# Performance work log

Measured on AMD Instinct MI355X. Metric: run time of the kernel, lower is better.

The kernel has to match this reference:

```python
import jax, jax.numpy as jnp
from jax import lax
import numpy as np

N3, N2, N1, N0 = 862, 1723, 3445, 6890  # mesh hierarchy (SMPL 6890 verts)
DEG, K = 16, 4  # nnz/row per Chebyshev support; K = order 3 + 1 supports


def _conv(x, w, b, s):
    y = lax.conv_general_dilated(x, w, (s, s), 'VALID', dimension_numbers=('NCHW', 'OIHW', 'NCHW'))
    return y + b[None, :, None, None]


def _pool(x):
    return lax.reduce_window(x, -jnp.inf, lax.max, (1, 1, 2, 2), (1, 1, 2, 2), 'VALID')


def _lin(x, w, b):
    return x @ w.T + b


def _rodrigues(r):  # [J,3] axis-angle -> [J,3,3] (batch_rodrigues)
    th = jnp.linalg.norm(r, axis=1, keepdims=True) + 1e-8
    k = r / th
    kx, ky, kz = k[:, 0], k[:, 1], k[:, 2]
    z = jnp.zeros_like(kx)
    Km = jnp.stack([z, -kz, ky, kz, z, -kx, -ky, kx, z], axis=1).reshape(-1, 3, 3)
    th = th[:, :, None]
    return jnp.eye(3, dtype=r.dtype)[None] + jnp.sin(th) * Km + (1.0 - jnp.cos(th)) * (Km @ Km)


def _spmm(idx, val, x):  # torch.sparse.mm with fixed nnz/row; idx,val: [N,D]
    return jnp.einsum('nd,ndf->nf', val, x[idx])


def _gcl(x, idx, val, W, b):  # Chebyshev graph conv: sum_k (A_k @ x) @ W_k + b
    return jnp.einsum('knd,kndf,kfo->no', val, x[idx], W) + b


def _basenet(frame, p):
    (c1w, c1b, c2w, c2b, c3w, c3b, c4w, c4b, c5w, c5b, fc1w, fc1b, fc4w, fc4b) = p
    c = _pool(jax.nn.relu(_conv(frame, c1w, c1b, 2)))
    c = _pool(jax.nn.relu(_conv(c, c2w, c2b, 1)))
    c = _pool(jax.nn.relu(_conv(c, c3w, c3b, 1)))
    c = _pool(jax.nn.relu(_conv(c, c4w, c4b, 1)))
    c = _pool(_conv(c, c5w, c5b, 1))  # [1,128,14,14]
    flat = jnp.transpose(c, (0, 3, 2, 1)).reshape(1, -1)  # torch.transpose(c,1,-1).reshape(1,-1)
    return _lin(flat, fc1w, fc1b), jax.nn.relu(_lin(flat, fc4w, fc4b))


def _forward(segmentations, poses, pose_mean, trans,
             c1w, c1b, c2w, c2b, c3w, c3b, c4w, c4b, c5w, c5b,
             fc1w, fc1b, fc2w, fc2b, fc3w, fc3b, fc4w, fc4b,
             fc5w, fc5b, fc6w, fc6b, fc7w, fc7b,
             gW3, gb3, gW2, gb2, gW1, gb1, gW0, gb0,
             av3, av2, av1, av0, uv2, uv1, uv0,
             ai3, ai2, ai1, ai0, ui2, ui1, ui0):
    nf = segmentations.shape[0]
    bp = (c1w, c1b, c2w, c2b, c3w, c3b, c4w, c4b, c5w, c5b, fc1w, fc1b, fc4w, fc4b)
    shape20, pose200 = jax.vmap(lambda f: _basenet(f, bp))(segmentations)  # [F,1,20],[F,1,200]
    pose_feat = jax.nn.relu(_lin(poses, fc5w, fc5b))  # [F,1,200]
    cat = jnp.concatenate([pose200, pose_feat], axis=-1)  # [F,1,400]
    pose_results = _lin(_lin(cat, fc6w, fc6b), fc7w, fc7b)  # [F,1,219]
    pm = pose_mean.at[:3].set(0.0)
    pose_init = _rodrigues(pm.reshape(-1, 3)).reshape(-1)  # [216]
    pct = jnp.concatenate([trans, pose_init])[None, None]  # [1,1,219]
    add = pose_results + pct
    add_poses = add[..., 3:].reshape(nf, -1, 24, 3, 3)
    add_trans = add[..., :3]
    betas_avr = shape20.reshape(-1, 20).mean(0)  # [20]
    betas_val = _lin(betas_avr, fc3w, fc3b)[None]  # [1,10]
    x = _lin(betas_avr, fc2w, fc2b).reshape(N3, 64)
    x = jax.nn.relu(_gcl(x, ai3, av3, gW3, gb3))  # [862,32]
    x = _spmm(ui2, uv2, x)                         # [1723,32]
    x = jax.nn.relu(_gcl(x, ai2, av2, gW2, gb2))  # [1723,16]
    x = _spmm(ui1, uv1, x)                         # [3445,16]
    x = jax.nn.relu(_gcl(x, ai1, av1, gW1, gb1))  # [3445,16]
    x = _spmm(ui0, uv0, x)                         # [6890,16]
    x = jnp.tanh(_gcl(x, ai0, av0, gW0, gb0))     # [6890,3]
    offsets = (x / 10.0)[None]
    return offsets, betas_val, add_poses, add_trans


def setup_inputs():
    ks = iter(jax.random.split(jax.random.key(0), 80))
    f32 = jnp.float32
    nrm = lambda shp, s: jax.random.normal(next(ks), shp, f32) * s
    uni = lambda shp, s: jax.random.uniform(next(ks), shp, f32) * s
    ri = lambda shp, hi: jax.random.randint(next(ks), shp, 0, hi)
    inp = {}
    inp['segmentations'] = nrm((8, 1, 3, 1017, 1017), 1.0)
    inp['poses'] = nrm((8, 1, 75), 1.0)
    inp['pose_mean'] = nrm((72,), 0.3)
    inp['trans'] = jnp.array([0.0, 0.2, -2.3], f32)
    for nm, shp, s in [('c1w', (8, 3, 3, 3), .1), ('c1b', (8,), .01), ('c2w', (16, 8, 3, 3), .1), ('c2b', (16,), .01),
                       ('c3w', (32, 16, 3, 3), .1), ('c3b', (32,), .01), ('c4w', (64, 32, 3, 3), .1), ('c4b', (64,), .01),
                       ('c5w', (128, 64, 3, 3), .1), ('c5b', (128,), .01),
                       ('fc1w', (20, 25088), .01), ('fc1b', (20,), .01), ('fc2w', (55168, 20), .05), ('fc2b', (55168,), .01),
                       ('fc3w', (10, 20), .05), ('fc3b', (10,), .01), ('fc4w', (200, 25088), .01), ('fc4b', (200,), .01),
                       ('fc5w', (200, 75), .05), ('fc5b', (200,), .01), ('fc6w', (100, 400), .05), ('fc6b', (100,), .01),
                       ('fc7w', (219, 100), .05), ('fc7b', (219,), .01),
                       ('gW3', (4, 64, 32), .1), ('gb3', (32,), .01), ('gW2', (4, 32, 16), .1), ('gb2', (16,), .01),
                       ('gW1', (4, 16, 16), .1), ('gb1', (16,), .01), ('gW0', (4, 16, 3), .1), ('gb0', (3,), .01)]:
        inp[nm] = nrm(shp, s)
    for nm, n in [('3', N3), ('2', N2), ('1', N1), ('0', N0)]:
        inp['av' + nm] = uni((K, n, DEG), 0.2)
        inp['ai' + nm] = ri((K, n, DEG), n)
    for nm, n_fine, n_coarse in [('2', N2, N3), ('1', N1, N2), ('0', N0, N1)]:
        inp['uv' + nm] = uni((n_fine, 4), 0.3)
        inp['ui' + nm] = ri((n_fine, 4), n_coarse)
    return inp


def reference(segmentations, poses, pose_mean, trans,
              c1w, c1b, c2w, c2b, c3w, c3b, c4w, c4b, c5w, c5b,
              fc1w, fc1b, fc2w, fc2b, fc3w, fc3b, fc4w, fc4b,
              fc5w, fc5b, fc6w, fc6b, fc7w, fc7b,
              gW3, gb3, gW2, gb2, gW1, gb1, gW0, gb0,
              av3, av2, av1, av0, uv2, uv1, uv0,
              ai3, ai2, ai1, ai0, ui2, ui1, ui0):
    return _forward(segmentations, poses, pose_mean, trans,
                    c1w, c1b, c2w, c2b, c3w, c3b, c4w, c4b, c5w, c5b,
                    fc1w, fc1b, fc2w, fc2b, fc3w, fc3b, fc4w, fc4b,
                    fc5w, fc5b, fc6w, fc6b, fc7w, fc7b,
                    gW3, gb3, gW2, gb2, gW1, gb1, gW0, gb0,
                    av3, av2, av1, av0, uv2, uv1, uv0,
                    ai3, ai2, ai1, ai0, ui2, ui1, ui0)
```

## Files before the change

kernel.cpp:

```cpp
#include <hip/hip_runtime.h>
#include <math.h>

__global__ __launch_bounds__(256) void conv1_lds(
    const float* __restrict__ in, const float* __restrict__ w,
    const float* __restrict__ bias, float* __restrict__ out)
{
    constexpr int Hin = 1017, P = 254;
    __shared__ float li[17][4][65];
    const int f  = blockIdx.y;
    const int ct = blockIdx.x & 3;
    const int rt = blockIdx.x >> 2;
    const int t  = threadIdx.x;
    const int lane = t & 63, wid = t >> 6;
    const int row0 = rt * 16, col0 = ct * 256;
    const float* inf = in + (size_t)f * 3 * Hin * Hin;

    const int ph = rt * 4 + wid, pw = ct * 64 + lane;
    const bool wactive = (ph < P) && (pw < P);

    float acc[32];
    #pragma unroll
    for (int i = 0; i < 32; i++) acc[i] = 0.f;

    for (int ic = 0; ic < 3; ic++) {
        __syncthreads();
        const float* src = inf + (size_t)ic * Hin * Hin;
        #pragma unroll
        for (int i = 0; i < 17; i++) {
            int gr = row0 + i; if (gr > Hin - 1) gr = Hin - 1;
            int gc = col0 + t; if (gc > Hin - 1) gc = Hin - 1;
            li[i][t & 3][t >> 2] = src[(size_t)gr * Hin + gc];
        }
        if (t < 17) {
            int gr = row0 + t; if (gr > Hin - 1) gr = Hin - 1;
            int gc = col0 + 256; if (gc > Hin - 1) gc = Hin - 1;
            li[t][0][64] = src[(size_t)gr * Hin + gc];
        }
        __syncthreads();

        float win[25];
        #pragma unroll
        for (int r = 0; r < 5; r++)
            #pragma unroll
            for (int c = 0; c < 5; c++)
                win[r * 5 + c] = li[4 * wid + r][c & 3][lane + (c >> 2)];

        #pragma unroll
        for (int oc = 0; oc < 8; oc++) {
            float wr[9];
            #pragma unroll
            for (int j = 0; j < 9; j++) wr[j] = w[(oc * 3 + ic) * 9 + j];
            #pragma unroll
            for (int py = 0; py < 2; py++)
                #pragma unroll
                for (int px = 0; px < 2; px++) {
                    float s = acc[(oc * 2 + py) * 2 + px];
                    #pragma unroll
                    for (int kh = 0; kh < 3; kh++)
                        #pragma unroll
                        for (int kw = 0; kw < 3; kw++)
                            s += wr[kh * 3 + kw] * win[(2 * py + kh) * 5 + (2 * px + kw)];
                    acc[(oc * 2 + py) * 2 + px] = s;
                }
        }
    }

    if (wactive) {
        #pragma unroll
        for (int oc = 0; oc < 8; oc++) {
            float m = fmaxf(fmaxf(acc[oc * 4 + 0], acc[oc * 4 + 1]),
                            fmaxf(acc[oc * 4 + 2], acc[oc * 4 + 3]));
            m = fmaxf(m + bias[oc], 0.f);
            out[(((size_t)f * 8 + oc) * P + ph) * P + pw] = m;
        }
    }
}

template<int IC, int OCG, bool RELU, bool FLATOUT>
__global__ __launch_bounds__(256) void conv_pool_s1(
    const float* __restrict__ in, const float* __restrict__ w,
    const float* __restrict__ bias, float* __restrict__ out,
    int Hin, int P, int OC)
{
    const int f = blockIdx.y, g = blockIdx.z;
    int tid = blockIdx.x * 256 + threadIdx.x;
    if (tid >= P * P) return;
    int ph = tid / P, pw = tid % P;
    const float* inf = in + ((size_t)f * IC) * Hin * Hin + (size_t)(2 * ph) * Hin + 2 * pw;
    const float* wg = w + (size_t)g * OCG * IC * 9;

    float acc[OCG * 4];
    #pragma unroll
    for (int i = 0; i < OCG * 4; i++) acc[i] = 0.f;

    for (int ic = 0; ic < IC; ic++) {
        const float* p = inf + (size_t)ic * Hin * Hin;
        float win[4][4];
        #pragma unroll
        for (int r = 0; r < 4; r++) {
            float2 a = *(const float2*)(p + (size_t)r * Hin);
            float2 b = *(const float2*)(p + (size_t)r * Hin + 2);
            win[r][0] = a.x; win[r][1] = a.y; win[r][2] = b.x; win[r][3] = b.y;
        }
        #pragma unroll
        for (int oc = 0; oc < OCG; oc++) {
            float wr[9];
            #pragma unroll
            for (int j = 0; j < 9; j++) wr[j] = wg[(oc * IC + ic) * 9 + j];
            #pragma unroll
            for (int py = 0; py < 2; py++)
                #pragma unroll
                for (int px = 0; px < 2; px++) {
                    float s = acc[(oc * 2 + py) * 2 + px];
                    #pragma unroll
                    for (int kh = 0; kh < 3; kh++)
                        #pragma unroll
                        for (int kw = 0; kw < 3; kw++)
                            s += wr[kh * 3 + kw] * win[py + kh][px + kw];
                    acc[(oc * 2 + py) * 2 + px] = s;
                }
        }
    }

    #pragma unroll
    for (int oc = 0; oc < OCG; oc++) {
        float m = fmaxf(fmaxf(acc[oc * 4 + 0], acc[oc * 4 + 1]),
                        fmaxf(acc[oc * 4 + 2], acc[oc * 4 + 3]));
        m += bias[g * OCG + oc];
        if (RELU) m = fmaxf(m, 0.f);
        int ocg = g * OCG + oc;
        if (FLATOUT) {
            out[(size_t)f * (P * P * OC) + (pw * P + ph) * OC + ocg] = m;
        } else {
            out[(((size_t)f * OC + ocg) * P + ph) * P + pw] = m;
        }
    }
}

__global__ __launch_bounds__(256) void fc_head_plus(
    const float* __restrict__ flat,
    const float* __restrict__ fc1w, const float* __restrict__ fc1b,
    const float* __restrict__ fc4w, const float* __restrict__ fc4b,
    const float* __restrict__ poses,
    const float* __restrict__ fc5w, const float* __restrict__ fc5b,
    float* __restrict__ shape20, float* __restrict__ pose200,
    float* __restrict__ pose_feat)
{
    int o = blockIdx.x;
    if (o < 220) {
        const float* W = (o < 20) ? fc1w + (size_t)o * 25088
                                  : fc4w + (size_t)(o - 20) * 25088;
        const float4* W4  = (const float4*)W;
        const float4* fl4 = (const float4*)flat;
        float acc[8];
        #pragma unroll
        for (int f = 0; f < 8; f++) acc[f] = 0.f;
        for (int i = threadIdx.x; i < 6272; i += 256) {
            float4 wv = W4[i];
            #pragma unroll
            for (int f = 0; f < 8; f++) {
                float4 xv = fl4[f * 6272 + i];
                acc[f] += wv.x * xv.x + wv.y * xv.y + wv.z * xv.z + wv.w * xv.w;
            }
        }
        #pragma unroll
        for (int f = 0; f < 8; f++)
            for (int off = 32; off > 0; off >>= 1)
                acc[f] += __shfl_down(acc[f], off, 64);
        __shared__ float red[4][8];
        int wid = threadIdx.x >> 6, lane = threadIdx.x & 63;
        if (lane == 0) {
            #pragma unroll
            for (int f = 0; f < 8; f++) red[wid][f] = acc[f];
        }
        __syncthreads();
        if (threadIdx.x < 8) {
            int f = threadIdx.x;
            float s = red[0][f] + red[1][f] + red[2][f] + red[3][f];
            if (o < 20) shape20[f * 20 + o] = s + fc1b[o];
            else        pose200[f * 200 + (o - 20)] = fmaxf(s + fc4b[o - 20], 0.f);
        }
    } else {
        int t = (o - 220) * 256 + threadIdx.x;
        if (t >= 8 * 200) return;
        int f = t / 200, oo = t % 200;
        float s = fc5b[oo];
        const float* pr = poses + f * 75;
        const float* wr = fc5w + oo * 75;
        #pragma unroll 5
        for (int j = 0; j < 75; j++) s += pr[j] * wr[j];
        pose_feat[f * 200 + oo] = fmaxf(s, 0.f);
    }
}

__global__ __launch_bounds__(256) void mid_fused(
    const float* __restrict__ shape20,
    const float* __restrict__ fc2w, const float* __restrict__ fc2b,
    const float* __restrict__ fc3w, const float* __restrict__ fc3b,
    float* __restrict__ x0, float* __restrict__ out,
    const float* __restrict__ pose200, const float* __restrict__ pose_feat,
    const float* __restrict__ fc6w, const float* __restrict__ fc6b,
    float* __restrict__ t1)
{
    int b = blockIdx.x, t = threadIdx.x;
    if (b < 216) {
        __shared__ float avr[20];
        if (t < 20) {
            float s = 0.f;
            for (int f = 0; f < 8; f++) s += shape20[f * 20 + t];
            avr[t] = s * 0.125f;
        }
        __syncthreads();
        int r = b * 256 + t;
        if (r < 55168) {
            float s = fc2b[r];
            const float4* w4 = (const float4*)(fc2w + (size_t)r * 20);
            #pragma unroll
            for (int q = 0; q < 5; q++) {
                float4 wv = w4[q];
                s += wv.x * avr[q * 4 + 0] + wv.y * avr[q * 4 + 1]
                   + wv.z * avr[q * 4 + 2] + wv.w * avr[q * 4 + 3];
            }
            x0[r] = s;
        }
        if (b == 0 && t < 10) {
            float s = fc3b[t];
            for (int j = 0; j < 20; j++) s += fc3w[t * 20 + j] * avr[j];
            out[20670 + t] = s;
        }
    } else {
        int wv = (b - 216) * 4 + (t >> 6);
        int lane = t & 63;
        if (wv >= 8 * 100) return;
        int f = wv / 100, o = wv % 100;
        float s = 0.f;
        for (int j = lane; j < 400; j += 64) {
            float xv = (j < 200) ? pose200[f * 200 + j] : pose_feat[f * 200 + (j - 200)];
            s += xv * fc6w[o * 400 + j];
        }
        #pragma unroll
        for (int off = 32; off > 0; off >>= 1) s += __shfl_down(s, off, 64);
        if (lane == 0) t1[f * 100 + o] = s + fc6b[o];
    }
}

__global__ __launch_bounds__(256) void pose_fc7(
    const float* __restrict__ t1, const float* __restrict__ fc7w,
    const float* __restrict__ fc7b, const float* __restrict__ pose_mean,
    const float* __restrict__ trans, float* __restrict__ out)
{
    int wv = blockIdx.x * 4 + (threadIdx.x >> 6);
    int lane = threadIdx.x & 63;
    if (wv >= 8 * 219) return;
    int f = wv / 219, c = wv % 219;
    float s = 0.f;
    {
        float xv = t1[f * 100 + lane];
        s += xv * fc7w[c * 100 + lane];
        int j2 = lane + 64;
        if (j2 < 100) s += t1[f * 100 + j2] * fc7w[c * 100 + j2];
    }
    #pragma unroll
    for (int off = 32; off > 0; off >>= 1) s += __shfl_down(s, off, 64);
    if (lane != 0) return;
    s += fc7b[c];
    float pct;
    if (c < 3) {
        pct = trans[c];
    } else {
        int j = (c - 3) / 9, e = (c - 3) % 9;
        float rx = (j == 0) ? 0.f : pose_mean[3 * j + 0];
        float ry = (j == 0) ? 0.f : pose_mean[3 * j + 1];
        float rz = (j == 0) ? 0.f : pose_mean[3 * j + 2];
        float th = sqrtf(rx * rx + ry * ry + rz * rz) + 1e-8f;
        float kx = rx / th, ky = ry / th, kz = rz / th;
        float sn = sinf(th), c2 = 1.f - cosf(th);
        float R[9];
        R[0] = 1.f - c2 * (ky * ky + kz * kz);
        R[1] = -sn * kz + c2 * (kx * ky);
        R[2] =  sn * ky + c2 * (kx * kz);
        R[3] =  sn * kz + c2 * (kx * ky);
        R[4] = 1.f - c2 * (kx * kx + kz * kz);
        R[5] = -sn * kx + c2 * (ky * kz);
        R[6] = -sn * ky + c2 * (kx * kz);
        R[7] =  sn * kx + c2 * (ky * kz);
        R[8] = 1.f - c2 * (kx * kx + ky * ky);
        pct = R[e];
    }
    s += pct;
    if (c < 3) out[22408 + f * 3 + c] = s;
    else       out[20680 + f * 216 + (c - 3)] = s;
}

template<int F, int O, int ACT>
__global__ __launch_bounds__(256) void gcl(
    const float* __restrict__ x, const int* __restrict__ ai,
    const float* __restrict__ av, const float* __restrict__ gW,
    const float* __restrict__ gb, float* __restrict__ y, int N)
{
    constexpr int VPW = 64 / F;
    constexpr int VPB = 4 * VPW;
    constexpr int HS  = 4 * F + 8;
    __shared__ float h[VPB][HS];

    int wid = threadIdx.x >> 6, lane = threadIdx.x & 63;
    {
        int vl = wid * VPW + (VPW == 1 ? 0 : lane / F);
        int fl = lane % F;
        int n = blockIdx.x * VPB + vl;
        if (n < N) {
            #pragma unroll
            for (int k = 0; k < 4; k++) {
                const int*   ip = ai + ((size_t)k * N + n) * 16;
                const float* vp = av + ((size_t)k * N + n) * 16;
                float s = 0.f;
                #pragma unroll
                for (int d = 0; d < 16; d++)
                    s += vp[d] * x[(size_t)ip[d] * F + fl];
                h[vl][k * F + fl] = s;
            }
        }
    }
    __syncthreads();

    int t = threadIdx.x;
    if (t < VPB * O) {
        int vl = t / O, o = t % O;
        int n = blockIdx.x * VPB + vl;
        if (n < N) {
            float s = gb[o];
            #pragma unroll
            for (int k = 0; k < 4; k++)
                for (int f2 = 0; f2 < F; f2++)
                    s += h[vl][k * F + f2] * gW[((size_t)k * F + f2) * O + o];
            if (ACT == 0) s = fmaxf(s, 0.f);
            else          s = tanhf(s) * 0.1f;
            y[(size_t)n * O + o] = s;
        }
    }
}

template<int F>
__global__ __launch_bounds__(256) void spmm(
    const float* __restrict__ x, const int* __restrict__ ui,
    const float* __restrict__ uv, float* __restrict__ y, int N)
{
    int t = blockIdx.x * 256 + threadIdx.x;
    if (t >= N * F) return;
    int n = t / F, f = t % F;
    float s = 0.f;
    #pragma unroll
    for (int j = 0; j < 4; j++)
        s += uv[n * 4 + j] * x[(size_t)ui[n * 4 + j] * F + f];
    y[t] = s;
}

extern "C" void kernel_launch(void* const* d_in, const int* in_sizes, int n_in,
                              void* d_out, int out_size, void* d_ws, size_t ws_size,
                              hipStream_t stream) {
    (void)in_sizes; (void)n_in; (void)out_size; (void)ws_size;

    const float* seg   = (const float*)d_in[0];
    const float* poses = (const float*)d_in[1];
    const float* pmean = (const float*)d_in[2];
    const float* trans = (const float*)d_in[3];
    const float* c1w = (const float*)d_in[4];  const float* c1b = (const float*)d_in[5];
    const float* c2w = (const float*)d_in[6];  const float* c2b = (const float*)d_in[7];
    const float* c3w = (const float*)d_in[8];  const float* c3b = (const float*)d_in[9];
    const float* c4w = (const float*)d_in[10]; const float* c4b = (const float*)d_in[11];
    const float* c5w = (const float*)d_in[12]; const float* c5b = (const float*)d_in[13];
    const float* fc1w = (const float*)d_in[14]; const float* fc1b = (const float*)d_in[15];
    const float* fc2w = (const float*)d_in[16]; const float* fc2b = (const float*)d_in[17];
    const float* fc3w = (const float*)d_in[18]; const float* fc3b = (const float*)d_in[19];
    const float* fc4w = (const float*)d_in[20]; const float* fc4b = (const float*)d_in[21];
    const float* fc5w = (const float*)d_in[22]; const float* fc5b = (const float*)d_in[23];
    const float* fc6w = (const float*)d_in[24]; const float* fc6b = (const float*)d_in[25];
    const float* fc7w = (const float*)d_in[26]; const float* fc7b = (const float*)d_in[27];
    const float* gW3 = (const float*)d_in[28]; const float* gb3 = (const float*)d_in[29];
    const float* gW2 = (const float*)d_in[30]; const float* gb2 = (const float*)d_in[31];
    const float* gW1 = (const float*)d_in[32]; const float* gb1 = (const float*)d_in[33];
    const float* gW0 = (const float*)d_in[34]; const float* gb0 = (const float*)d_in[35];
    const float* av3 = (const float*)d_in[36]; const int* ai3 = (const int*)d_in[37];
    const float* av2 = (const float*)d_in[38]; const int* ai2 = (const int*)d_in[39];
    const float* av1 = (const float*)d_in[40]; const int* ai1 = (const int*)d_in[41];
    const float* av0 = (const float*)d_in[42]; const int* ai0 = (const int*)d_in[43];
    const float* uv2 = (const float*)d_in[44]; const int* ui2 = (const int*)d_in[45];
    const float* uv1 = (const float*)d_in[46]; const int* ui1 = (const int*)d_in[47];
    const float* uv0 = (const float*)d_in[48]; const int* ui0 = (const int*)d_in[49];

    float* W = (float*)d_ws;
    float* out = (float*)d_out;

    float* pool1 = W + 0;
    float* pool2 = W + 4129024;
    float* pool3 = W + 0;
    float* pool4 = W + 4129024;
    float* flat5 = W + 4589824;
    float* shape20 = W + 1000000;
    float* pose200 = shape20 + 160;
    float* x0  = pose200 + 1600;
    float* y3  = x0 + 55168;
    float* x2  = y3 + 27584;
    float* y2  = x2 + 55136;
    float* x1  = y2 + 27568;
    float* y1  = x1 + 55120;
    float* x0u = y1 + 55120;
    float* pose_feat = x0u + 110240;
    float* t1 = pose_feat + 1600;

    conv1_lds<<<dim3(256, 8), 256, 0, stream>>>(seg, c1w, c1b, pool1);
    conv_pool_s1<8, 8, true, false>
        <<<dim3(63, 8, 2), 256, 0, stream>>>(pool1, c2w, c2b, pool2, 254, 126, 16);
    conv_pool_s1<16, 8, true, false>
        <<<dim3(16, 8, 4), 256, 0, stream>>>(pool2, c3w, c3b, pool3, 126, 62, 32);
    conv_pool_s1<32, 4, true, false>
        <<<dim3(4, 8, 16), 256, 0, stream>>>(pool3, c4w, c4b, pool4, 62, 30, 64);
    conv_pool_s1<64, 2, false, true>
        <<<dim3(1, 8, 64), 256, 0, stream>>>(pool4, c5w, c5b, flat5, 30, 14, 128);

    fc_head_plus<<<dim3(227), 256, 0, stream>>>(flat5, fc1w, fc1b, fc4w, fc4b,
                                                poses, fc5w, fc5b,
                                                shape20, pose200, pose_feat);
    mid_fused<<<dim3(416), 256, 0, stream>>>(shape20, fc2w, fc2b, fc3w, fc3b, x0, out,
                                             pose200, pose_feat, fc6w, fc6b, t1);
    pose_fc7<<<dim3(438), 256, 0, stream>>>(t1, fc7w, fc7b, pmean, trans, out);

    gcl<64, 32, 0><<<dim3(216),  256, 0, stream>>>(x0,  ai3, av3, gW3, gb3, y3, 862);
    spmm<32>      <<<dim3(216),  256, 0, stream>>>(y3,  ui2, uv2, x2, 1723);
    gcl<32, 16, 0><<<dim3(216),  256, 0, stream>>>(x2,  ai2, av2, gW2, gb2, y2, 1723);
    spmm<16>      <<<dim3(216),  256, 0, stream>>>(y2,  ui1, uv1, x1, 3445);
    gcl<16, 16, 0><<<dim3(216),  256, 0, stream>>>(x1,  ai1, av1, gW1, gb1, y1, 3445);
    spmm<16>      <<<dim3(431),  256, 0, stream>>>(y1,  ui0, uv0, x0u, 6890);
    gcl<16, 3, 1> <<<dim3(431),  256, 0, stream>>>(x0u, ai0, av0, gW0, gb0, out, 6890);
}
```

Measured before the change: 170.0 us.

## Fuse upsampling spmm into graph convs and merge fc7 with first GCL

Removes the three standalone upsample spmm kernels. Each graph-conv layer now computes the upsampled input on the fly by gathering through the upsample indices inside its neighbor loop. The fc7 pose head is merged with the first graph conv layer into one launch using block-index dispatch. Conv3 and conv4 launches also change their per-block output-channel grouping. Together these cut launch count and intermediate buffer traffic. In exchange, each fused layer recomputes each upsampled vertex about 16 times per support, so it does more gathers.

```diff
diff --git a/kernel.cpp b/kernel.cpp
--- a/kernel.cpp
+++ b/kernel.cpp
@@ -244,57 +244,93 @@
     }
 }
 
-__global__ __launch_bounds__(256) void pose_fc7(
+__global__ __launch_bounds__(256) void fc7_gcl3(
+    const float* __restrict__ x0, const int* __restrict__ ai3,
+    const float* __restrict__ av3, const float* __restrict__ gW3,
+    const float* __restrict__ gb3, float* __restrict__ y3,
     const float* __restrict__ t1, const float* __restrict__ fc7w,
     const float* __restrict__ fc7b, const float* __restrict__ pose_mean,
     const float* __restrict__ trans, float* __restrict__ out)
 {
-    int wv = blockIdx.x * 4 + (threadIdx.x >> 6);
-    int lane = threadIdx.x & 63;
-    if (wv >= 8 * 219) return;
-    int f = wv / 219, c = wv % 219;
-    float s = 0.f;
-    {
-        float xv = t1[f * 100 + lane];
-        s += xv * fc7w[c * 100 + lane];
+    constexpr int F = 64, O = 32, N = 862;
+    constexpr int VPB = 4;
+    constexpr int HS = 4 * F + 8;
+    __shared__ float h[VPB][HS];
+    const int b = blockIdx.x;
+    const int wid = threadIdx.x >> 6, lane = threadIdx.x & 63;
+
+    if (b < 216) {
+        int n = b * VPB + wid;
+        if (n < N) {
+            #pragma unroll
+            for (int k = 0; k < 4; k++) {
+                const int*   ip = ai3 + ((size_t)k * N + n) * 16;
+                const float* vp = av3 + ((size_t)k * N + n) * 16;
+                float s = 0.f;
+                #pragma unroll
+                for (int d = 0; d < 16; d++)
+                    s += vp[d] * x0[(size_t)ip[d] * F + lane];
+                h[wid][k * F + lane] = s;
+            }
+        }
+        __syncthreads();
+        int t = threadIdx.x;
+        if (t < VPB * O) {
+            int vl = t / O, o = t % O;
+            int n2 = b * VPB + vl;
+            if (n2 < N) {
+                float s = gb3[o];
+                #pragma unroll
+                for (int k = 0; k < 4; k++)
+                    for (int f2 = 0; f2 < F; f2++)
+                        s += h[vl][k * F + f2] * gW3[((size_t)k * F + f2) * O + o];
+                y3[(size_t)n2 * O + o] = fmaxf(s, 0.f);
+            }
+        }
+    } else {
+        int wv = (b - 216) * 4 + wid;
+        if (wv >= 8 * 219) return;
+        int f = wv / 219, c = wv % 219;
+        float s = t1[f * 100 + lane] * fc7w[c * 100 + lane];
         int j2 = lane + 64;
         if (j2 < 100) s += t1[f * 100 + j2] * fc7w[c * 100 + j2];
-    }
-    #pragma unroll
-    for (int off = 32; off > 0; off >>= 1) s += __shfl_down(s, off, 64);
-    if (lane != 0) return;
-    s += fc7b[c];
-    float pct;
-    if (c < 3) {
-        pct = trans[c];
-    } else {
-        int j = (c - 3) / 9, e = (c - 3) % 9;
-        float rx = (j == 0) ? 0.f : pose_mean[3 * j + 0];
-        float ry = (j == 0) ? 0.f : pose_mean[3 * j + 1];
-        float rz = (j == 0) ? 0.f : pose_mean[3 * j + 2];
-        float th = sqrtf(rx * rx + ry * ry + rz * rz) + 1e-8f;
-        float kx = rx / th, ky = ry / th, kz = rz / th;
-        float sn = sinf(th), c2 = 1.f - cosf(th);
-        float R[9];
-        R[0] = 1.f - c2 * (ky * ky + kz * kz);
-        R[1] = -sn * kz + c2 * (kx * ky);
-        R[2] =  sn * ky + c2 * (kx * kz);
-        R[3] =  sn * kz + c2 * (kx * ky);
-        R[4] = 1.f - c2 * (kx * kx + kz * kz);
-        R[5] = -sn * kx + c2 * (ky * kz);
-        R[6] = -sn * ky + c2 * (kx * kz);
-        R[7] =  sn * kx + c2 * (ky * kz);
-        R[8] = 1.f - c2 * (kx * kx + ky * ky);
-        pct = R[e];
-    }
-    s += pct;
-    if (c < 3) out[22408 + f * 3 + c] = s;
-    else       out[20680 + f * 216 + (c - 3)] = s;
+        #pragma unroll
+        for (int off = 32; off > 0; off >>= 1) s += __shfl_down(s, off, 64);
+        if (lane != 0) return;
+        s += fc7b[c];
+        float pct;
+        if (c < 3) {
+            pct = trans[c];
+        } else {
+            int j = (c - 3) / 9, e = (c - 3) % 9;
+            float rx = (j == 0) ? 0.f : pose_mean[3 * j + 0];
+            float ry = (j == 0) ? 0.f : pose_mean[3 * j + 1];
+            float rz = (j == 0) ? 0.f : pose_mean[3 * j + 2];
+            float th = sqrtf(rx * rx + ry * ry + rz * rz) + 1e-8f;
+            float kx = rx / th, ky = ry / th, kz = rz / th;
+            float sn = sinf(th), c2 = 1.f - cosf(th);
+            float R[9];
+            R[0] = 1.f - c2 * (ky * ky + kz * kz);
+            R[1] = -sn * kz + c2 * (kx * ky);
+            R[2] =  sn * ky + c2 * (kx * kz);
+            R[3] =  sn * kz + c2 * (kx * ky);
+            R[4] = 1.f - c2 * (kx * kx + kz * kz);
+            R[5] = -sn * kx + c2 * (ky * kz);
+            R[6] = -sn * ky + c2 * (kx * kz);
+            R[7] =  sn * kx + c2 * (ky * kz);
+            R[8] = 1.f - c2 * (kx * kx + ky * ky);
+            pct = R[e];
+        }
+        s += pct;
+        if (c < 3) out[22408 + f * 3 + c] = s;
+        else       out[20680 + f * 216 + (c - 3)] = s;
+    }
 }
 
 template<int F, int O, int ACT>
-__global__ __launch_bounds__(256) void gcl(
-    const float* __restrict__ x, const int* __restrict__ ai,
+__global__ __launch_bounds__(256) void gcl_up(
+    const float* __restrict__ y_prev, const int* __restrict__ ui,
+    const float* __restrict__ uv, const int* __restrict__ ai,
     const float* __restrict__ av, const float* __restrict__ gW,
     const float* __restrict__ gb, float* __restrict__ y, int N)
 {
@@ -315,8 +351,16 @@
                 const float* vp = av + ((size_t)k * N + n) * 16;
                 float s = 0.f;
                 #pragma unroll
-                for (int d = 0; d < 16; d++)
-                    s += vp[d] * x[(size_t)ip[d] * F + fl];
+                for (int d = 0; d < 16; d++) {
+                    int m = ip[d];
+                    const int*   up = ui + (size_t)m * 4;
+                    const float* wp = uv + (size_t)m * 4;
+                    float xv = wp[0] * y_prev[(size_t)up[0] * F + fl]
+                             + wp[1] * y_prev[(size_t)up[1] * F + fl]
+                             + wp[2] * y_prev[(size_t)up[2] * F + fl]
+                             + wp[3] * y_prev[(size_t)up[3] * F + fl];
+                    s += vp[d] * xv;
+                }
                 h[vl][k * F + fl] = s;
             }
         }
@@ -338,21 +382,6 @@
             y[(size_t)n * O + o] = s;
         }
     }
-}
-
-template<int F>
-__global__ __launch_bounds__(256) void spmm(
-    const float* __restrict__ x, const int* __restrict__ ui,
-    const float* __restrict__ uv, float* __restrict__ y, int N)
-{
-    int t = blockIdx.x * 256 + threadIdx.x;
-    if (t >= N * F) return;
-    int n = t / F, f = t % F;
-    float s = 0.f;
-    #pragma unroll
-    for (int j = 0; j < 4; j++)
-        s += uv[n * 4 + j] * x[(size_t)ui[n * 4 + j] * F + f];
-    y[t] = s;
 }
 
 extern "C" void kernel_launch(void* const* d_in, const int* in_sizes, int n_in,
@@ -400,21 +429,18 @@
     float* pose200 = shape20 + 160;
     float* x0  = pose200 + 1600;
     float* y3  = x0 + 55168;
-    float* x2  = y3 + 27584;
-    float* y2  = x2 + 55136;
-    float* x1  = y2 + 27568;
-    float* y1  = x1 + 55120;
-    float* x0u = y1 + 55120;
-    float* pose_feat = x0u + 110240;
+    float* y2  = y3 + 27584;
+    float* y1  = y2 + 27568;
+    float* pose_feat = y1 + 55120;
     float* t1 = pose_feat + 1600;
 
     conv1_lds<<<dim3(256, 8), 256, 0, stream>>>(seg, c1w, c1b, pool1);
     conv_pool_s1<8, 8, true, false>
         <<<dim3(63, 8, 2), 256, 0, stream>>>(pool1, c2w, c2b, pool2, 254, 126, 16);
-    conv_pool_s1<16, 8, true, false>
-        <<<dim3(16, 8, 4), 256, 0, stream>>>(pool2, c3w, c3b, pool3, 126, 62, 32);
-    conv_pool_s1<32, 4, true, false>
-        <<<dim3(4, 8, 16), 256, 0, stream>>>(pool3, c4w, c4b, pool4, 62, 30, 64);
+    conv_pool_s1<16, 4, true, false>
+        <<<dim3(16, 8, 8), 256, 0, stream>>>(pool2, c3w, c3b, pool3, 126, 62, 32);
+    conv_pool_s1<32, 2, true, false>
+        <<<dim3(4, 8, 32), 256, 0, stream>>>(pool3, c4w, c4b, pool4, 62, 30, 64);
     conv_pool_s1<64, 2, false, true>
         <<<dim3(1, 8, 64), 256, 0, stream>>>(pool4, c5w, c5b, flat5, 30, 14, 128);
 
@@ -423,13 +449,10 @@
                                                 shape20, pose200, pose_feat);
     mid_fused<<<dim3(416), 256, 0, stream>>>(shape20, fc2w, fc2b, fc3w, fc3b, x0, out,
                                              pose200, pose_feat, fc6w, fc6b, t1);
-    pose_fc7<<<dim3(438), 256, 0, stream>>>(t1, fc7w, fc7b, pmean, trans, out);
-
-    gcl<64, 32, 0><<<dim3(216),  256, 0, stream>>>(x0,  ai3, av3, gW3, gb3, y3, 862);
-    spmm<32>      <<<dim3(216),  256, 0, stream>>>(y3,  ui2, uv2, x2, 1723);
-    gcl<32, 16, 0><<<dim3(216),  256, 0, stream>>>(x2,  ai2, av2, gW2, gb2, y2, 1723);
-    spmm<16>      <<<dim3(216),  256, 0, stream>>>(y2,  ui1, uv1, x1, 3445);
-    gcl<16, 16, 0><<<dim3(216),  256, 0, stream>>>(x1,  ai1, av1, gW1, gb1, y1, 3445);
-    spmm<16>      <<<dim3(431),  256, 0, stream>>>(y1,  ui0, uv0, x0u, 6890);
-    gcl<16, 3, 1> <<<dim3(431),  256, 0, stream>>>(x0u, ai0, av0, gW0, gb0, out, 6890);
-}
+
+    fc7_gcl3<<<dim3(654), 256, 0, stream>>>(x0, ai3, av3, gW3, gb3, y3,
+                                            t1, fc7w, fc7b, pmean, trans, out);
+    gcl_up<32, 16, 0><<<dim3(216), 256, 0, stream>>>(y3, ui2, uv2, ai2, av2, gW2, gb2, y2, 1723);
+    gcl_up<16, 16, 0><<<dim3(216), 256, 0, stream>>>(y2, ui1, uv1, ai1, av1, gW1, gb1, y1, 3445);
+    gcl_up<16, 3, 1> <<<dim3(431), 256, 0, stream>>>(y1, ui0, uv0, ai0, av0, gW0, gb0, out, 6890);
+}
```

Result: slower. 266.4 us (+56.6%).
